# Kernel tuning notes

Measured on AMD Instinct MI355X. Metric: run time of the kernel, lower is better.

Reference implementation:

```python
import jax, jax.numpy as jnp
import numpy as np

B = 1024
IN_DIM = 165
COND = 150
EMB = 150
MB_OUT = 10
MB_INT = 50
FEAT = IN_DIM + EMB  # 315

def _w(key, shape, fan_in):
    return jax.random.normal(key, shape, dtype=jnp.float32) / np.float32(np.sqrt(fan_in))

def setup_inputs() -> dict:
    key = jax.random.key(0)
    ks = jax.random.split(key, 10)
    return {
        "time_series": jax.random.normal(ks[0], (B, IN_DIM), dtype=jnp.float32),
        "condition": jax.random.randint(ks[1], (B,), 0, COND, dtype=jnp.int64) if jax.config.jax_enable_x64 else jax.random.randint(ks[1], (B,), 0, COND, dtype=jnp.int32),
        "emb": jax.random.normal(ks[2], (COND, EMB), dtype=jnp.float32),
        "T": jax.random.normal(ks[3], (FEAT, MB_OUT, MB_INT), dtype=jnp.float32),
        "W1": _w(ks[4], (FEAT + MB_OUT, 1536), FEAT + MB_OUT),
        "b1": jnp.zeros((1536,), jnp.float32),
        "W2": _w(ks[5], (1536, 1024), 1536),
        "b2": jnp.zeros((1024,), jnp.float32),
        "W3": _w(ks[6], (1024, 512), 1024),
        "b3": jnp.zeros((512,), jnp.float32),
        "W4": _w(ks[7], (512, 256), 512),
        "b4": jnp.zeros((256,), jnp.float32),
        "W5": _w(ks[8], (256, 1), 256),
        "b5": jnp.zeros((1,), jnp.float32),
    }

def reference(time_series, condition, emb, T, W1, b1, W2, b2, W3, b3, W4, b4, W5, b5):
    # embedding lookup + concat -> x: [B, 315]
    y = emb[condition]
    x = jnp.concatenate([time_series, y], axis=1)
    # minibatch discrimination: M: [B, out, inter]
    M = jnp.einsum('bf,fok->bok', x, T)
    # pairwise L1 over intermediate dim -> [B, B, out]
    abs_diff = jnp.sum(jnp.abs(M[:, None, :, :] - M[None, :, :, :]), axis=3)
    mb_feats = jnp.exp(-abs_diff).sum(axis=1)  # [B, out] (includes self term exp(0)=1)
    h = jnp.concatenate([x, mb_feats], axis=1)  # [B, 325]
    lrelu = lambda v: jax.nn.leaky_relu(v, 0.2)
    h = lrelu(h @ W1 + b1)  # dropout is identity in eval mode
    h = lrelu(h @ W2 + b2)
    h = lrelu(h @ W3 + b3)
    h = lrelu(h @ W4 + b4)
    return jax.nn.sigmoid(h @ W5 + b5)  # [B, 1]
```

## Files before the change

### kernel.cpp

```cpp
#include <hip/hip_runtime.h>
#include <hip/hip_bf16.h>

#define B_N     1024
#define IN_DIM  165
#define EMB_D   150
#define FEAT    315
#define H0_W    325
#define H0_S    352
#define MB_OUT  10
#define MB_INT  50
#define MROW    64
#define NPROJ   12

typedef __attribute__((ext_vector_type(8))) short short8;
typedef __attribute__((ext_vector_type(4))) float f32x4;

__device__ __forceinline__ ushort f2bf(float f) {
    uint u = __float_as_uint(f);
    return (ushort)((u + 0x7fffu + ((u >> 16) & 1u)) >> 16);
}
__device__ __forceinline__ uint pack_split(float v) {
    ushort h = f2bf(v);
    float hf = __uint_as_float((uint)h << 16);
    ushort l = f2bf(v - hf);
    return (uint)h | ((uint)l << 16);
}
__device__ __forceinline__ float unpack_split(uint u) {
    return __uint_as_float(u << 16) + __uint_as_float(u & 0xffff0000u);
}

__global__ __launch_bounds__(320) void build_x_kernel(
    const float* __restrict__ ts, const int* __restrict__ cond,
    const float* __restrict__ emb, uint* __restrict__ h0p)
{
    int b = blockIdx.x, t = threadIdx.x;
    if (t < 37) h0p[b * H0_S + FEAT + t] = 0u;
    float v;
    if (t < IN_DIM)      v = ts[b * IN_DIM + t];
    else if (t < FEAT)   v = emb[cond[b] * EMB_D + (t - IN_DIM)];
    else return;
    h0p[b * H0_S + t] = pack_split(v);
}

__global__ __launch_bounds__(256) void pack_all_kernel(
    const float* __restrict__ T,  const float* __restrict__ W1,
    const float* __restrict__ W2, const float* __restrict__ W3,
    const float* __restrict__ W4, uint* __restrict__ Wp)
{
    int i = blockIdx.x * 256 + threadIdx.x;
    float v;
    if (i < 163840) {
        int k = i >> 9, n = i & 511;
        v = (k < FEAT && n < 500) ? T[k * 500 + n] : 0.f;
    } else if (i < 704512) {
        int j = i - 163840; int k = j / 1536, n = j - k * 1536;
        v = (k < H0_W) ? W1[k * 1536 + n] : 0.f;
    } else if (i < 2277376) {
        int j = i - 704512; v = W2[j];
    } else if (i < 2801664) {
        int j = i - 2277376; v = W3[j];
    } else if (i < 2932736) {
        int j = i - 2801664; v = W4[j];
    } else return;
    Wp[i] = pack_split(v);
}

template<int EPI, int PACKED>
__global__ __launch_bounds__(256) void gemm_mfma(
    const uint*  __restrict__ Ap, const void* __restrict__ Bw,
    const float* __restrict__ bias, void* __restrict__ Cout,
    int N, int K, int lda, int ldb, int ldc,
    int kIterTotal, int Ks, float* __restrict__ Pout)
{
    __shared__ ushort Ah[64 * 32], Al[64 * 32], Bh[64 * 32], Bl[64 * 32];

    const int t    = threadIdx.x;
    const int bm   = blockIdx.y << 6;
    const int bn   = blockIdx.x << 6;
    const int wid  = t >> 6, lane = t & 63;
    const int wm   = (wid >> 1) << 5, wn = (wid & 1) << 5;
    const int lm   = lane & 15, lc = lane >> 4;

    const int ar  = t >> 2, ac = t & 3;
    const int bn2 = t & 63, bk = t >> 6;

    const int z   = blockIdx.z;
    const int it0 = z * Ks;
    const int nIt = min(Ks, kIterTotal - it0);

    const int aw = ar  * 32 + ((ac ^ (ar  & 3)) << 3);
    const int bw = bn2 * 32 + ((bk ^ (bn2 & 3)) << 3);
    const int sw = (lc ^ (lm & 3)) << 3;
    const int a0 = (wm + lm)      * 32 + sw;
    const int a1 = (wm + 16 + lm) * 32 + sw;
    const int b0 = (wn + lm)      * 32 + sw;
    const int b1 = (wn + 16 + lm) * 32 + sw;

    uint curA[8], nxtA[8], curB[8], nxtB[8];

    auto loadA = [&](int k0, uint* dst) {
        const uint* p = Ap + (bm + ar) * lda + k0 + (ac << 3);
        uint4 v0 = *(const uint4*)p;
        uint4 v1 = *(const uint4*)(p + 4);
        dst[0] = v0.x; dst[1] = v0.y; dst[2] = v0.z; dst[3] = v0.w;
        dst[4] = v1.x; dst[5] = v1.y; dst[6] = v1.z; dst[7] = v1.w;
    };
    auto loadB = [&](int k0, uint* dst) {
        int kb = k0 + (bk << 3);
        if (PACKED) {
            const uint* p = (const uint*)Bw + kb * ldb + bn + bn2;
            #pragma unroll
            for (int j = 0; j < 8; ++j) dst[j] = p[j * ldb];
        } else {
            const float* p = (const float*)Bw + kb * ldb + bn + bn2;
            bool cok = (bn + bn2) < N;
            #pragma unroll
            for (int j = 0; j < 8; ++j)
                dst[j] = __float_as_uint((cok && (kb + j) < K) ? p[j * ldb] : 0.f);
        }
    };

    f32x4 acc[2][2] = {};

    loadA(it0 << 5, curA);
    loadB(it0 << 5, curB);

    for (int it = 0; it < nIt; ++it) {
        short8 vah, val, vbh, vbl;
        #pragma unroll
        for (int j = 0; j < 8; ++j) {
            uint ua = curA[j];
            vah[j] = (short)(ua & 0xffffu);
            val[j] = (short)(ua >> 16);
            if (PACKED) {
                uint ub = curB[j];
                vbh[j] = (short)(ub & 0xffffu);
                vbl[j] = (short)(ub >> 16);
            } else {
                float v = __uint_as_float(curB[j]);
                ushort h = f2bf(v);
                float hf = __uint_as_float((uint)h << 16);
                vbh[j] = (short)h;
                vbl[j] = (short)f2bf(v - hf);
            }
        }
        __syncthreads();
        *(short8*)&Ah[aw] = vah;
        *(short8*)&Al[aw] = val;
        *(short8*)&Bh[bw] = vbh;
        *(short8*)&Bl[bw] = vbl;
        __syncthreads();

        if (it + 1 < nIt) {
            loadA((it0 + it + 1) << 5, nxtA);
            loadB((it0 + it + 1) << 5, nxtB);
        }

        short8 fah0 = *(const short8*)&Ah[a0];
        short8 fah1 = *(const short8*)&Ah[a1];
        short8 fal0 = *(const short8*)&Al[a0];
        short8 fal1 = *(const short8*)&Al[a1];
        short8 fbh0 = *(const short8*)&Bh[b0];
        short8 fbh1 = *(const short8*)&Bh[b1];
        short8 fbl0 = *(const short8*)&Bl[b0];
        short8 fbl1 = *(const short8*)&Bl[b1];

        acc[0][0] = __builtin_amdgcn_mfma_f32_16x16x32_bf16(fah0, fbh0, acc[0][0], 0, 0, 0);
        acc[0][1] = __builtin_amdgcn_mfma_f32_16x16x32_bf16(fah0, fbh1, acc[0][1], 0, 0, 0);
        acc[1][0] = __builtin_amdgcn_mfma_f32_16x16x32_bf16(fah1, fbh0, acc[1][0], 0, 0, 0);
        acc[1][1] = __builtin_amdgcn_mfma_f32_16x16x32_bf16(fah1, fbh1, acc[1][1], 0, 0, 0);
        acc[0][0] = __builtin_amdgcn_mfma_f32_16x16x32_bf16(fah0, fbl0, acc[0][0], 0, 0, 0);
        acc[0][1] = __builtin_amdgcn_mfma_f32_16x16x32_bf16(fah0, fbl1, acc[0][1], 0, 0, 0);
        acc[1][0] = __builtin_amdgcn_mfma_f32_16x16x32_bf16(fah1, fbl0, acc[1][0], 0, 0, 0);
        acc[1][1] = __builtin_amdgcn_mfma_f32_16x16x32_bf16(fah1, fbl1, acc[1][1], 0, 0, 0);
        acc[0][0] = __builtin_amdgcn_mfma_f32_16x16x32_bf16(fal0, fbh0, acc[0][0], 0, 0, 0);
        acc[0][1] = __builtin_amdgcn_mfma_f32_16x16x32_bf16(fal0, fbh1, acc[0][1], 0, 0, 0);
        acc[1][0] = __builtin_amdgcn_mfma_f32_16x16x32_bf16(fal1, fbh0, acc[1][0], 0, 0, 0);
        acc[1][1] = __builtin_amdgcn_mfma_f32_16x16x32_bf16(fal1, fbh1, acc[1][1], 0, 0, 0);

        #pragma unroll
        for (int j = 0; j < 8; ++j) { curA[j] = nxtA[j]; curB[j] = nxtB[j]; }
    }

    if (gridDim.z > 1) {
        float* P = Pout + (size_t)z * B_N * N;
        #pragma unroll
        for (int mi = 0; mi < 2; ++mi)
        #pragma unroll
        for (int ni = 0; ni < 2; ++ni)
        #pragma unroll
        for (int r = 0; r < 4; ++r) {
            int row = bm + wm + mi * 16 + lc * 4 + r;
            int col = bn + wn + ni * 16 + lm;
            if (col < N) P[row * N + col] = acc[mi][ni][r];
        }
        return;
    }

    #pragma unroll
    for (int mi = 0; mi < 2; ++mi)
    #pragma unroll
    for (int ni = 0; ni < 2; ++ni)
    #pragma unroll
    for (int r = 0; r < 4; ++r) {
        int row = bm + wm + mi * 16 + lc * 4 + r;
        int col = bn + wn + ni * 16 + lm;
        float v = acc[mi][ni][r];
        if (EPI == 0) {
            v += bias[col];
            v = (v > 0.f) ? v : 0.2f * v;
            ((uint*)Cout)[row * ldc + col] = pack_split(v);
        } else {
            if (col < N) {
                int o = col / MB_INT, kk = col - o * MB_INT;
                ((float*)Cout)[(o * B_N + row) * MROW + kk] = v;
            }
        }
    }
}

__global__ __launch_bounds__(256) void epi_pack_kernel(
    const float* __restrict__ P, const float* __restrict__ bias,
    uint* __restrict__ outp, int n4, int S)
{
    const int c4 = blockIdx.x * 64 + (threadIdx.x & 63);
    const int r  = blockIdx.y * 4 + (threadIdx.x >> 6);
    const int idx = r * n4 + c4;
    const float4* P4 = (const float4*)P;
    float4 v = P4[idx];
    for (int s = 1; s < S; ++s) {
        float4 w = P4[(size_t)s * B_N * n4 + idx];
        v.x += w.x; v.y += w.y; v.z += w.z; v.w += w.w;
    }
    float4 bb = ((const float4*)bias)[c4];
    v.x += bb.x; v.y += bb.y; v.z += bb.z; v.w += bb.w;
    v.x = (v.x > 0.f) ? v.x : 0.2f * v.x;
    v.y = (v.y > 0.f) ? v.y : 0.2f * v.y;
    v.z = (v.z > 0.f) ? v.z : 0.2f * v.z;
    v.w = (v.w > 0.f) ? v.w : 0.2f * v.w;
    uint4 o;
    o.x = pack_split(v.x); o.y = pack_split(v.y);
    o.z = pack_split(v.z); o.w = pack_split(v.w);
    ((uint4*)outp)[idx] = o;
}

__global__ __launch_bounds__(256) void epi_m2_kernel(
    const float* __restrict__ P, float* __restrict__ M2, int S)
{
    int i = blockIdx.x * 256 + threadIdx.x;
    if (i >= B_N * 500) return;
    int r = i / 500, c = i - r * 500;
    float v = P[i];
    for (int s = 1; s < S; ++s) v += P[(size_t)s * B_N * 500 + i];
    int o = c / MB_INT, k = c - o * MB_INT;
    M2[(o * B_N + r) * MROW + k] = v;
}

__device__ __constant__ const unsigned long long PMASK[NPROJ] = {
    0x2B5F1E3A4B6C7DULL, 0x19D4A7C3E85B26ULL, 0x3E6A1D59F0B483ULL,
    0x07C2F8A135E9D6ULL, 0x2A94E6B7D01C3FULL, 0x35B8D2041A7E6CULL,
    0x1CE07B3F68A5D2ULL, 0x22F1A4C85D93E0ULL, 0x0B67D3E92C50F8ULL,
    0x38A0C5171E4B9DULL, 0x114E92F6A3D078ULL, 0x2D73B0E84F169AULL
};

template<int J0>
__device__ __forceinline__ void proj3(const float* __restrict__ row, float* s) {
    float s0 = 0.f, s1 = 0.f, s2 = 0.f;
    #pragma unroll
    for (int k = 0; k < MB_INT; ++k) {
        float v = row[k];
        if ((PMASK[J0]     >> k) & 1ULL) s0 -= v; else s0 += v;
        if ((PMASK[J0 + 4] >> k) & 1ULL) s1 -= v; else s1 += v;
        if ((PMASK[J0 + 8] >> k) & 1ULL) s2 -= v; else s2 += v;
    }
    s[0] = s0; s[1] = s1; s[2] = s2;
}

__global__ __launch_bounds__(256) void proj_kernel(
    const float* __restrict__ M2, float* __restrict__ Rproj)
{
    __shared__ float Ls[64 * 53];
    const int rt = blockIdx.x, o = blockIdx.y, t = threadIdx.x;

    #pragma unroll
    for (int i = 0; i < 13; ++i) {
        int idx = t + i * 256;
        int r = idx / 52, k = idx - r * 52;
        float v = (k < MB_INT) ? M2[(o * B_N + rt * 64 + r) * MROW + k] : 0.f;
        Ls[r * 53 + k] = v;
    }
    __syncthreads();

    const int r = t & 63, j0 = t >> 6;
    float s[3];
    if      (j0 == 0) proj3<0>(&Ls[r * 53], s);
    else if (j0 == 1) proj3<1>(&Ls[r * 53], s);
    else if (j0 == 2) proj3<2>(&Ls[r * 53], s);
    else              proj3<3>(&Ls[r * 53], s);

    float* dst = Rproj + (size_t)(o * B_N + rt * 64 + r) * NPROJ;
    dst[j0] = s[0]; dst[j0 + 4] = s[1]; dst[j0 + 8] = s[2];
}

__global__ __launch_bounds__(256) void pairwise_kernel(
    const float* __restrict__ M2, const float* __restrict__ Rproj,
    float* __restrict__ part)
{
    __shared__ float Lp[32 * NPROJ];
    const int grp = blockIdx.x, o = blockIdx.y, ch = blockIdx.z;
    const int t = threadIdx.x, wid = t >> 6, lane = t & 63;

    if (t < 96)
        ((float4*)Lp)[t] = ((const float4*)(Rproj + (size_t)(o * B_N + ch * 32) * NPROJ))[t];
    __syncthreads();

    const int b = (grp * 4 + wid) * 64 + lane;

    const float4* Ar = (const float4*)(M2 + (size_t)(o * B_N + b) * MROW);
    float4 A0 = Ar[0], A1 = Ar[1], A2 = Ar[2],  A3 = Ar[3];
    float4 A4 = Ar[4], A5 = Ar[5], A6 = Ar[6],  A7 = Ar[7];
    float4 A8 = Ar[8], A9 = Ar[9], A10 = Ar[10], A11 = Ar[11];
    float2 A12 = *(const float2*)((const float*)Ar + 48);

    const float4* Pr = (const float4*)(Rproj + (size_t)(o * B_N + b) * NPROJ);
    float4 P0 = Pr[0], P1 = Pr[1], P2 = Pr[2];

    const int selfstep = (ch == (b >> 5)) ? (b & 31) : -1;
    float acc = (selfstep >= 0) ? 1.f : 0.f;

    const float* Bbase = M2 + (size_t)(o * B_N + ch * 32) * MROW;

    for (int b2 = 0; b2 < 32; ++b2) {
        const float4* qp = (const float4*)&Lp[b2 * NPROJ];
        float4 q0 = qp[0], q1 = qp[1], q2 = qp[2];
        float d0 = fabsf(P0.x - q0.x), d1 = fabsf(P0.y - q0.y);
        float d2 = fabsf(P0.z - q0.z), d3 = fabsf(P0.w - q0.w);
        float d4 = fabsf(P1.x - q1.x), d5 = fabsf(P1.y - q1.y);
        float d6 = fabsf(P1.z - q1.z), d7 = fabsf(P1.w - q1.w);
        float d8 = fabsf(P2.x - q2.x), d9 = fabsf(P2.y - q2.y);
        float dA = fabsf(P2.z - q2.z), dB = fabsf(P2.w - q2.w);
        float m0 = fmaxf(fmaxf(d0, d1), fmaxf(d2, d3));
        float m1 = fmaxf(fmaxf(d4, d5), fmaxf(d6, d7));
        float m2 = fmaxf(fmaxf(d8, d9), fmaxf(dA, dB));
        float dmax = fmaxf(fmaxf(m0, m1), m2);

        if (__all(dmax > 110.f || b2 == selfstep)) continue;

        const float4* q = (const float4*)(Bbase + b2 * MROW);
        float4 s = {0.f, 0.f, 0.f, 0.f};
        float4 v;
        v = q[0];  s.x += fabsf(A0.x - v.x);  s.y += fabsf(A0.y - v.y);  s.z += fabsf(A0.z - v.z);  s.w += fabsf(A0.w - v.w);
        v = q[1];  s.x += fabsf(A1.x - v.x);  s.y += fabsf(A1.y - v.y);  s.z += fabsf(A1.z - v.z);  s.w += fabsf(A1.w - v.w);
        v = q[2];  s.x += fabsf(A2.x - v.x);  s.y += fabsf(A2.y - v.y);  s.z += fabsf(A2.z - v.z);  s.w += fabsf(A2.w - v.w);
        v = q[3];  s.x += fabsf(A3.x - v.x);  s.y += fabsf(A3.y - v.y);  s.z += fabsf(A3.z - v.z);  s.w += fabsf(A3.w - v.w);
        v = q[4];  s.x += fabsf(A4.x - v.x);  s.y += fabsf(A4.y - v.y);  s.z += fabsf(A4.z - v.z);  s.w += fabsf(A4.w - v.w);
        v = q[5];  s.x += fabsf(A5.x - v.x);  s.y += fabsf(A5.y - v.y);  s.z += fabsf(A5.z - v.z);  s.w += fabsf(A5.w - v.w);
        v = q[6];  s.x += fabsf(A6.x - v.x);  s.y += fabsf(A6.y - v.y);  s.z += fabsf(A6.z - v.z);  s.w += fabsf(A6.w - v.w);
        v = q[7];  s.x += fabsf(A7.x - v.x);  s.y += fabsf(A7.y - v.y);  s.z += fabsf(A7.z - v.z);  s.w += fabsf(A7.w - v.w);
        v = q[8];  s.x += fabsf(A8.x - v.x);  s.y += fabsf(A8.y - v.y);  s.z += fabsf(A8.z - v.z);  s.w += fabsf(A8.w - v.w);
        v = q[9];  s.x += fabsf(A9.x - v.x);  s.y += fabsf(A9.y - v.y);  s.z += fabsf(A9.z - v.z);  s.w += fabsf(A9.w - v.w);
        v = q[10]; s.x += fabsf(A10.x - v.x); s.y += fabsf(A10.y - v.y); s.z += fabsf(A10.z - v.z); s.w += fabsf(A10.w - v.w);
        v = q[11]; s.x += fabsf(A11.x - v.x); s.y += fabsf(A11.y - v.y); s.z += fabsf(A11.z - v.z); s.w += fabsf(A11.w - v.w);
        v = q[12]; s.x += fabsf(A12.x - v.x); s.y += fabsf(A12.y - v.y);
        float d = (s.x + s.y) + (s.z + s.w);
        float e = __expf(-d);
        acc += (b2 == selfstep) ? 0.f : e;
    }
    part[(ch * MB_OUT + o) * B_N + b] = acc;
}

__global__ __launch_bounds__(256) void mb_reduce_kernel(
    const float* __restrict__ part, uint* __restrict__ h0p)
{
    int i = blockIdx.x * 256 + threadIdx.x;
    if (i < MB_OUT * B_N) {
        int o = i / B_N, b = i - o * B_N;
        float s = 0.f;
        #pragma unroll
        for (int ch = 0; ch < 32; ++ch)
            s += part[(ch * MB_OUT + o) * B_N + b];
        h0p[b * H0_S + FEAT + o] = pack_split(s);
    }
}

__global__ __launch_bounds__(256) void final_kernel(
    const uint* __restrict__ h4p, const float* __restrict__ W5,
    const float* __restrict__ b5, float* __restrict__ out)
{
    const int wave = threadIdx.x >> 6;
    const int lane = threadIdx.x & 63;
    const int row  = blockIdx.x * 4 + wave;

    const uint4  h = ((const uint4*)(h4p + row * 256))[lane];
    const float4 w = ((const float4*)W5)[lane];
    float s = unpack_split(h.x) * w.x + unpack_split(h.y) * w.y
            + unpack_split(h.z) * w.z + unpack_split(h.w) * w.w;
    #pragma unroll
    for (int off = 32; off > 0; off >>= 1)
        s += __shfl_xor(s, off);
    if (lane == 0) {
        float z = s + b5[0];
        out[row] = 1.f / (1.f + __expf(-z));
    }
}

extern "C" void kernel_launch(void* const* d_in, const int* in_sizes, int n_in,
                              void* d_out, int out_size, void* d_ws, size_t ws_size,
                              hipStream_t stream)
{
    const float* ts   = (const float*)d_in[0];
    const int*   cond = (const int*)  d_in[1];
    const float* emb  = (const float*)d_in[2];
    const float* T    = (const float*)d_in[3];
    const float* W1   = (const float*)d_in[4];
    const float* b1   = (const float*)d_in[5];
    const float* W2   = (const float*)d_in[6];
    const float* b2   = (const float*)d_in[7];
    const float* W3   = (const float*)d_in[8];
    const float* b3   = (const float*)d_in[9];
    const float* W4   = (const float*)d_in[10];
    const float* b4   = (const float*)d_in[11];
    const float* W5   = (const float*)d_in[12];
    const float* b5   = (const float*)d_in[13];
    float* out = (float*)d_out;

    uint*  h0p  = (uint*)d_ws;
    float* M2   = (float*)(h0p + 360448);
    uint*  h1p  = (uint*)(M2 + 655360);
    uint*  h2p  = h1p + 1572864;
    uint*  h3p  = (uint*)M2;
    uint*  h4p  = h1p;
    float* part  = (float*)h1p;
    float* Rproj = part + 327680;
    const size_t baseU = 360448 + 655360 + 1572864 + 1048576;

    uint* Wpk = (uint*)d_ws + baseU;
    uint* Tp  = Wpk;
    uint* W1p = Tp  + 163840;
    uint* W2p = W1p + 540672;
    uint* W3p = W2p + 1572864;
    uint* W4p = W3p + 524288;
    const size_t packU = 2932736;
    const bool packed = (ws_size / 4) >= (baseU + packU);

    const size_t pbase = packed ? baseU + packU : baseU;
    size_t capU = (ws_size / 4 > pbase) ? ws_size / 4 - pbase : 0;
    float* Pbuf = (float*)((uint*)d_ws + pbase);

    auto fits = [&](int s, int N) { return (size_t)s * B_N * N <= capU; };
    const int ST = fits(2, 500)  ? 2 : 1;
    const int S1 = fits(2, 1536) ? 2 : 1;
    const int S2 = fits(3, 1024) ? 3 : (fits(2, 1024) ? 2 : 1);
    const int S3 = fits(4, 512)  ? 4 : (fits(2, 512)  ? 2 : 1);
    const int S4 = fits(4, 256)  ? 4 : (fits(2, 256)  ? 2 : 1);

    if (packed)
        pack_all_kernel<<<(2932736 + 255) / 256, 256, 0, stream>>>(T, W1, W2, W3, W4, Wpk);

    build_x_kernel<<<B_N, 320, 0, stream>>>(ts, cond, emb, h0p);

    {
        int kit = 10, ks = (kit + ST - 1) / ST;
        dim3 g(8, 16, ST);
        if (packed)
            gemm_mfma<1,1><<<g, 256, 0, stream>>>(h0p, Tp, nullptr, M2,
                                                  500, FEAT, H0_S, 512, 0, kit, ks, Pbuf);
        else
            gemm_mfma<1,0><<<g, 256, 0, stream>>>(h0p, T, nullptr, M2,
                                                  500, FEAT, H0_S, 500, 0, kit, ks, Pbuf);
        if (ST > 1)
            epi_m2_kernel<<<(B_N * 500 + 255) / 256, 256, 0, stream>>>(Pbuf, M2, ST);
    }

    { dim3 g(16, MB_OUT); proj_kernel<<<g, 256, 0, stream>>>(M2, Rproj); }
    { dim3 g(4, MB_OUT, 32); pairwise_kernel<<<g, 256, 0, stream>>>(M2, Rproj, part); }
    mb_reduce_kernel<<<(MB_OUT * B_N + 255) / 256, 256, 0, stream>>>(part, h0p);

    auto runL = [&](const uint* in, const float* Wf, const uint* Wp,
                    const float* bia, uint* outp, int N, int K, int lda,
                    int kit, int ldbp, int S) {
        int ks = (kit + S - 1) / S;
        dim3 g(N / 64, 16, S);
        if (packed)
            gemm_mfma<0,1><<<g, 256, 0, stream>>>(in, Wp, bia, outp, N, K, lda, ldbp, N, kit, ks, Pbuf);
        else
            gemm_mfma<0,0><<<g, 256, 0, stream>>>(in, Wf, bia, outp, N, K, lda, N,  N, kit, ks, Pbuf);
        if (S > 1) {
            dim3 ge((N / 4) / 64, B_N / 4);
            epi_pack_kernel<<<ge, 256, 0, stream>>>(Pbuf, bia, outp, N / 4, S);
        }
    };

    runL(h0p, W1, W1p, b1, h1p, 1536, H0_W, H0_S, 11, 1536, S1);
    runL(h1p, W2, W2p, b2, h2p, 1024, 1536, 1536, 48, 1024, S2);
    runL(h2p, W3, W3p, b3, h3p,  512, 1024, 1024, 32,  512, S3);
    runL(h3p, W4, W4p, b4, h4p,  256,  512,  512, 16,  256, S4);

    final_kernel<<<B_N / 4, 256, 0, stream>>>(h4p, W5, b5, out);
}
```

Before: 109.1 us.

## Drop low-bf16 weight term in MLP GEMMs and fuse input prep into one kernel

```diff
diff --git a/kernel.cpp b/kernel.cpp
--- a/kernel.cpp
+++ b/kernel.cpp
@@ -42,27 +42,46 @@
     h0p[b * H0_S + t] = pack_split(v);
 }
 
-__global__ __launch_bounds__(256) void pack_all_kernel(
-    const float* __restrict__ T,  const float* __restrict__ W1,
-    const float* __restrict__ W2, const float* __restrict__ W3,
-    const float* __restrict__ W4, uint* __restrict__ Wp)
+__global__ __launch_bounds__(256) void prep_kernel(
+    const float* __restrict__ ts, const int* __restrict__ cond,
+    const float* __restrict__ emb, const float* __restrict__ T,
+    const float* __restrict__ W1, const float* __restrict__ W2,
+    const float* __restrict__ W3, const float* __restrict__ W4,
+    uint* __restrict__ h0p, uint* __restrict__ Tp, uint* __restrict__ Wb)
 {
     int i = blockIdx.x * 256 + threadIdx.x;
-    float v;
     if (i < 163840) {
         int k = i >> 9, n = i & 511;
-        v = (k < FEAT && n < 500) ? T[k * 500 + n] : 0.f;
-    } else if (i < 704512) {
-        int j = i - 163840; int k = j / 1536, n = j - k * 1536;
-        v = (k < H0_W) ? W1[k * 1536 + n] : 0.f;
-    } else if (i < 2277376) {
-        int j = i - 704512; v = W2[j];
-    } else if (i < 2801664) {
-        int j = i - 2277376; v = W3[j];
-    } else if (i < 2932736) {
-        int j = i - 2801664; v = W4[j];
-    } else return;
-    Wp[i] = pack_split(v);
+        float v = (k < FEAT && n < 500) ? T[k * 500 + n] : 0.f;
+        Tp[i] = pack_split(v);
+    } else if (i < 1548288) {
+        int j = i - 163840;
+        float v0 = 0.f, v1 = 0.f;
+        if (j < 270336) {
+            int k = j / 768, n = (j - k * 768) * 2;
+            if (k < H0_W) { v0 = W1[k * 1536 + n]; v1 = W1[k * 1536 + n + 1]; }
+        } else if (j < 1056768) {
+            int jj = j - 270336;
+            int k = jj >> 9, n = (jj & 511) * 2;
+            v0 = W2[k * 1024 + n]; v1 = W2[k * 1024 + n + 1];
+        } else if (j < 1318912) {
+            int jj = j - 1056768;
+            int k = jj >> 8, n = (jj & 255) * 2;
+            v0 = W3[k * 512 + n]; v1 = W3[k * 512 + n + 1];
+        } else {
+            int jj = j - 1318912;
+            int k = jj >> 7, n = (jj & 127) * 2;
+            v0 = W4[k * 256 + n]; v1 = W4[k * 256 + n + 1];
+        }
+        Wb[j] = (uint)f2bf(v0) | ((uint)f2bf(v1) << 16);
+    } else if (i < 1908736) {
+        int j = i - 1548288;
+        int b = j / H0_S, c = j - b * H0_S;
+        uint o = 0u;
+        if (c < IN_DIM)    o = pack_split(ts[b * IN_DIM + c]);
+        else if (c < FEAT) o = pack_split(emb[cond[b] * EMB_D + (c - IN_DIM)]);
+        h0p[b * H0_S + c] = o;
+    }
 }
 
 template<int EPI, int PACKED>
@@ -182,21 +201,6 @@
         for (int j = 0; j < 8; ++j) { curA[j] = nxtA[j]; curB[j] = nxtB[j]; }
     }
 
-    if (gridDim.z > 1) {
-        float* P = Pout + (size_t)z * B_N * N;
-        #pragma unroll
-        for (int mi = 0; mi < 2; ++mi)
-        #pragma unroll
-        for (int ni = 0; ni < 2; ++ni)
-        #pragma unroll
-        for (int r = 0; r < 4; ++r) {
-            int row = bm + wm + mi * 16 + lc * 4 + r;
-            int col = bn + wn + ni * 16 + lm;
-            if (col < N) P[row * N + col] = acc[mi][ni][r];
-        }
-        return;
-    }
-
     #pragma unroll
     for (int mi = 0; mi < 2; ++mi)
     #pragma unroll
@@ -219,6 +223,126 @@
     }
 }
 
+__global__ __launch_bounds__(256) void gemm_mfma2(
+    const uint* __restrict__ Ap, const ushort* __restrict__ Bw,
+    const float* __restrict__ bias, uint* __restrict__ Cout,
+    int N, int lda, int ldb, int ldc,
+    int kIterTotal, int Ks, float* __restrict__ Pout)
+{
+    __shared__ ushort Ah[64 * 32], Al[64 * 32], Bh[64 * 32];
+
+    const int t    = threadIdx.x;
+    const int bm   = blockIdx.y << 6;
+    const int bn   = blockIdx.x << 6;
+    const int wid  = t >> 6, lane = t & 63;
+    const int wm   = (wid >> 1) << 5, wn = (wid & 1) << 5;
+    const int lm   = lane & 15, lc = lane >> 4;
+
+    const int ar  = t >> 2, ac = t & 3;
+    const int bn2 = t & 63, bk = t >> 6;
+
+    const int z   = blockIdx.z;
+    const int it0 = z * Ks;
+    const int nIt = min(Ks, kIterTotal - it0);
+
+    const int aw = ar  * 32 + ((ac ^ (ar  & 3)) << 3);
+    const int bw = bn2 * 32 + ((bk ^ (bn2 & 3)) << 3);
+    const int sw = (lc ^ (lm & 3)) << 3;
+    const int a0 = (wm + lm)      * 32 + sw;
+    const int a1 = (wm + 16 + lm) * 32 + sw;
+    const int b0 = (wn + lm)      * 32 + sw;
+    const int b1 = (wn + 16 + lm) * 32 + sw;
+
+    uint   curA[8], nxtA[8];
+    ushort curB[8], nxtB[8];
+
+    auto loadA = [&](int k0, uint* dst) {
+        const uint* p = Ap + (bm + ar) * lda + k0 + (ac << 3);
+        uint4 v0 = *(const uint4*)p;
+        uint4 v1 = *(const uint4*)(p + 4);
+        dst[0] = v0.x; dst[1] = v0.y; dst[2] = v0.z; dst[3] = v0.w;
+        dst[4] = v1.x; dst[5] = v1.y; dst[6] = v1.z; dst[7] = v1.w;
+    };
+    auto loadB = [&](int k0, ushort* dst) {
+        const ushort* p = Bw + (k0 + (bk << 3)) * ldb + bn + bn2;
+        #pragma unroll
+        for (int j = 0; j < 8; ++j) dst[j] = p[j * ldb];
+    };
+
+    f32x4 acc[2][2] = {};
+
+    loadA(it0 << 5, curA);
+    loadB(it0 << 5, curB);
+
+    for (int it = 0; it < nIt; ++it) {
+        short8 vah, val, vbh;
+        #pragma unroll
+        for (int j = 0; j < 8; ++j) {
+            uint ua = curA[j];
+            vah[j] = (short)(ua & 0xffffu);
+            val[j] = (short)(ua >> 16);
+            vbh[j] = (short)curB[j];
+        }
+        __syncthreads();
+        *(short8*)&Ah[aw] = vah;
+        *(short8*)&Al[aw] = val;
+        *(short8*)&Bh[bw] = vbh;
+        __syncthreads();
+
+        if (it + 1 < nIt) {
+            loadA((it0 + it + 1) << 5, nxtA);
+            loadB((it0 + it + 1) << 5, nxtB);
+        }
+
+        short8 fah0 = *(const short8*)&Ah[a0];
+        short8 fah1 = *(const short8*)&Ah[a1];
+        short8 fal0 = *(const short8*)&Al[a0];
+        short8 fal1 = *(const short8*)&Al[a1];
+        short8 fbh0 = *(const short8*)&Bh[b0];
+        short8 fbh1 = *(const short8*)&Bh[b1];
+
+        acc[0][0] = __builtin_amdgcn_mfma_f32_16x16x32_bf16(fah0, fbh0, acc[0][0], 0, 0, 0);
+        acc[0][1] = __builtin_amdgcn_mfma_f32_16x16x32_bf16(fah0, fbh1, acc[0][1], 0, 0, 0);
+        acc[1][0] = __builtin_amdgcn_mfma_f32_16x16x32_bf16(fah1, fbh0, acc[1][0], 0, 0, 0);
+        acc[1][1] = __builtin_amdgcn_mfma_f32_16x16x32_bf16(fah1, fbh1, acc[1][1], 0, 0, 0);
+        acc[0][0] = __builtin_amdgcn_mfma_f32_16x16x32_bf16(fal0, fbh0, acc[0][0], 0, 0, 0);
+        acc[0][1] = __builtin_amdgcn_mfma_f32_16x16x32_bf16(fal0, fbh1, acc[0][1], 0, 0, 0);
+        acc[1][0] = __builtin_amdgcn_mfma_f32_16x16x32_bf16(fal1, fbh0, acc[1][0], 0, 0, 0);
+        acc[1][1] = __builtin_amdgcn_mfma_f32_16x16x32_bf16(fal1, fbh1, acc[1][1], 0, 0, 0);
+
+        #pragma unroll
+        for (int j = 0; j < 8; ++j) { curA[j] = nxtA[j]; curB[j] = nxtB[j]; }
+    }
+
+    if (gridDim.z > 1) {
+        float* P = Pout + (size_t)z * B_N * N;
+        #pragma unroll
+        for (int mi = 0; mi < 2; ++mi)
+        #pragma unroll
+        for (int ni = 0; ni < 2; ++ni)
+        #pragma unroll
+        for (int r = 0; r < 4; ++r) {
+            int row = bm + wm + mi * 16 + lc * 4 + r;
+            int col = bn + wn + ni * 16 + lm;
+            P[row * N + col] = acc[mi][ni][r];
+        }
+        return;
+    }
+
+    #pragma unroll
+    for (int mi = 0; mi < 2; ++mi)
+    #pragma unroll
+    for (int ni = 0; ni < 2; ++ni)
+    #pragma unroll
+    for (int r = 0; r < 4; ++r) {
+        int row = bm + wm + mi * 16 + lc * 4 + r;
+        int col = bn + wn + ni * 16 + lm;
+        float v = acc[mi][ni][r] + bias[col];
+        v = (v > 0.f) ? v : 0.2f * v;
+        Cout[row * ldc + col] = pack_split(v);
+    }
+}
+
 __global__ __launch_bounds__(256) void epi_pack_kernel(
     const float* __restrict__ P, const float* __restrict__ bias,
     uint* __restrict__ outp, int n4, int S)
@@ -242,18 +366,6 @@
     o.x = pack_split(v.x); o.y = pack_split(v.y);
     o.z = pack_split(v.z); o.w = pack_split(v.w);
     ((uint4*)outp)[idx] = o;
-}
-
-__global__ __launch_bounds__(256) void epi_m2_kernel(
-    const float* __restrict__ P, float* __restrict__ M2, int S)
-{
-    int i = blockIdx.x * 256 + threadIdx.x;
-    if (i >= B_N * 500) return;
-    int r = i / 500, c = i - r * 500;
-    float v = P[i];
-    for (int s = 1; s < S; ++s) v += P[(size_t)s * B_N * 500 + i];
-    int o = c / MB_INT, k = c - o * MB_INT;
-    M2[(o * B_N + r) * MROW + k] = v;
 }
 
 __device__ __constant__ const unsigned long long PMASK[NPROJ] = {
@@ -434,67 +546,64 @@
     float* Rproj = part + 327680;
     const size_t baseU = 360448 + 655360 + 1572864 + 1048576;
 
-    uint* Wpk = (uint*)d_ws + baseU;
-    uint* Tp  = Wpk;
-    uint* W1p = Tp  + 163840;
-    uint* W2p = W1p + 540672;
-    uint* W3p = W2p + 1572864;
-    uint* W4p = W3p + 524288;
-    const size_t packU = 2932736;
+    uint* Tp = (uint*)d_ws + baseU;
+    uint* Wb = Tp + 163840;
+    ushort* W1b = (ushort*)Wb;
+    ushort* W2b = W1b + 540672;
+    ushort* W3b = W2b + 1572864;
+    ushort* W4b = W3b + 524288;
+    const size_t packU = 163840 + 1384448;
     const bool packed = (ws_size / 4) >= (baseU + packU);
 
     const size_t pbase = packed ? baseU + packU : baseU;
     size_t capU = (ws_size / 4 > pbase) ? ws_size / 4 - pbase : 0;
     float* Pbuf = (float*)((uint*)d_ws + pbase);
 
-    auto fits = [&](int s, int N) { return (size_t)s * B_N * N <= capU; };
-    const int ST = fits(2, 500)  ? 2 : 1;
-    const int S1 = fits(2, 1536) ? 2 : 1;
-    const int S2 = fits(3, 1024) ? 3 : (fits(2, 1024) ? 2 : 1);
-    const int S3 = fits(4, 512)  ? 4 : (fits(2, 512)  ? 2 : 1);
-    const int S4 = fits(4, 256)  ? 4 : (fits(2, 256)  ? 2 : 1);
-
-    if (packed)
-        pack_all_kernel<<<(2932736 + 255) / 256, 256, 0, stream>>>(T, W1, W2, W3, W4, Wpk);
-
-    build_x_kernel<<<B_N, 320, 0, stream>>>(ts, cond, emb, h0p);
-
-    {
-        int kit = 10, ks = (kit + ST - 1) / ST;
-        dim3 g(8, 16, ST);
-        if (packed)
-            gemm_mfma<1,1><<<g, 256, 0, stream>>>(h0p, Tp, nullptr, M2,
-                                                  500, FEAT, H0_S, 512, 0, kit, ks, Pbuf);
-        else
-            gemm_mfma<1,0><<<g, 256, 0, stream>>>(h0p, T, nullptr, M2,
-                                                  500, FEAT, H0_S, 500, 0, kit, ks, Pbuf);
-        if (ST > 1)
-            epi_m2_kernel<<<(B_N * 500 + 255) / 256, 256, 0, stream>>>(Pbuf, M2, ST);
-    }
-
-    { dim3 g(16, MB_OUT); proj_kernel<<<g, 256, 0, stream>>>(M2, Rproj); }
-    { dim3 g(4, MB_OUT, 32); pairwise_kernel<<<g, 256, 0, stream>>>(M2, Rproj, part); }
-    mb_reduce_kernel<<<(MB_OUT * B_N + 255) / 256, 256, 0, stream>>>(part, h0p);
-
-    auto runL = [&](const uint* in, const float* Wf, const uint* Wp,
-                    const float* bia, uint* outp, int N, int K, int lda,
-                    int kit, int ldbp, int S) {
-        int ks = (kit + S - 1) / S;
-        dim3 g(N / 64, 16, S);
-        if (packed)
-            gemm_mfma<0,1><<<g, 256, 0, stream>>>(in, Wp, bia, outp, N, K, lda, ldbp, N, kit, ks, Pbuf);
-        else
-            gemm_mfma<0,0><<<g, 256, 0, stream>>>(in, Wf, bia, outp, N, K, lda, N,  N, kit, ks, Pbuf);
-        if (S > 1) {
-            dim3 ge((N / 4) / 64, B_N / 4);
-            epi_pack_kernel<<<ge, 256, 0, stream>>>(Pbuf, bia, outp, N / 4, S);
-        }
-    };
-
-    runL(h0p, W1, W1p, b1, h1p, 1536, H0_W, H0_S, 11, 1536, S1);
-    runL(h1p, W2, W2p, b2, h2p, 1024, 1536, 1536, 48, 1024, S2);
-    runL(h2p, W3, W3p, b3, h3p,  512, 1024, 1024, 32,  512, S3);
-    runL(h3p, W4, W4p, b4, h4p,  256,  512,  512, 16,  256, S4);
+    if (packed) {
+        prep_kernel<<<7456, 256, 0, stream>>>(ts, cond, emb, T, W1, W2, W3, W4,
+                                              h0p, Tp, Wb);
+
+        { dim3 g(8, 16); gemm_mfma<1,1><<<g, 256, 0, stream>>>(
+              h0p, Tp, nullptr, M2, 500, FEAT, H0_S, 512, 0, 10, 10, Pbuf); }
+
+        { dim3 g(16, MB_OUT); proj_kernel<<<g, 256, 0, stream>>>(M2, Rproj); }
+        { dim3 g(4, MB_OUT, 32); pairwise_kernel<<<g, 256, 0, stream>>>(M2, Rproj, part); }
+        mb_reduce_kernel<<<(MB_OUT * B_N + 255) / 256, 256, 0, stream>>>(part, h0p);
+
+        { dim3 g(24, 16); gemm_mfma2<<<g, 256, 0, stream>>>(
+              h0p, W1b, b1, h1p, 1536, H0_S, 1536, 1536, 11, 11, Pbuf); }
+
+        {
+            int S2 = ((size_t)2 * B_N * 1024 <= capU) ? 2 : 1;
+            dim3 g(16, 16, S2);
+            gemm_mfma2<<<g, 256, 0, stream>>>(
+                h1p, W2b, b2, h2p, 1024, 1536, 1024, 1024, 48, (48 + S2 - 1) / S2, Pbuf);
+            if (S2 > 1) {
+                dim3 ge(4, 256);
+                epi_pack_kernel<<<ge, 256, 0, stream>>>(Pbuf, b2, h2p, 256, S2);
+            }
+        }
+
+        { dim3 g(8, 16); gemm_mfma2<<<g, 256, 0, stream>>>(
+              h2p, W3b, b3, h3p, 512, 1024, 512, 512, 32, 32, Pbuf); }
+        { dim3 g(4, 16); gemm_mfma2<<<g, 256, 0, stream>>>(
+              h3p, W4b, b4, h4p, 256, 512, 256, 256, 16, 16, Pbuf); }
+    } else {
+        build_x_kernel<<<B_N, 320, 0, stream>>>(ts, cond, emb, h0p);
+        { dim3 g(8, 16); gemm_mfma<1,0><<<g, 256, 0, stream>>>(
+              h0p, T, nullptr, M2, 500, FEAT, H0_S, 500, 0, 10, 10, Pbuf); }
+        { dim3 g(16, MB_OUT); proj_kernel<<<g, 256, 0, stream>>>(M2, Rproj); }
+        { dim3 g(4, MB_OUT, 32); pairwise_kernel<<<g, 256, 0, stream>>>(M2, Rproj, part); }
+        mb_reduce_kernel<<<(MB_OUT * B_N + 255) / 256, 256, 0, stream>>>(part, h0p);
+        { dim3 g(24, 16); gemm_mfma<0,0><<<g, 256, 0, stream>>>(
+              h0p, W1, b1, h1p, 1536, H0_W, H0_S, 1536, 1536, 11, 11, Pbuf); }
+        { dim3 g(16, 16); gemm_mfma<0,0><<<g, 256, 0, stream>>>(
+              h1p, W2, b2, h2p, 1024, 1536, 1536, 1024, 1024, 48, 48, Pbuf); }
+        { dim3 g(8, 16);  gemm_mfma<0,0><<<g, 256, 0, stream>>>(
+              h2p, W3, b3, h3p, 512, 1024, 1024, 512, 512, 32, 32, Pbuf); }
+        { dim3 g(4, 16);  gemm_mfma<0,0><<<g, 256, 0, stream>>>(
+              h3p, W4, b4, h4p, 256, 512, 512, 256, 256, 16, 16, Pbuf); }
+    }
 
     final_kernel<<<B_N / 4, 256, 0, stream>>>(h4p, W5, b5, out);
 }
```

New measurement: 118.3 us. +8.4%, slower.
